# Kernel optimization log

Hardware: AMD Instinct MI355X
Metric: run time of the kernel (lower is better)

Reference implementation:

```python
import jax, jax.numpy as jnp
import numpy as np

IMG, P, D, E, TOPK, H = 224, 14, 512, 10, 2, 8
NP = (IMG // P) ** 2  # 256 patches
PD = P * P            # 196
HID = 256             # expert hidden (hardcoded in source)


def _moe_layer(x, Wip, bip, Wqkv, bqkv, Wo, bo, Wg, bg, W1, b1, W2, b2):
    # input projection (input_dim == adjusted_dim == 512 here)
    h = x @ Wip + bip                                  # [b, s, d]
    b, s, d = h.shape
    hd = d // H
    # torch nn.MultiheadAttention with batch_first=False receives [b, s, d]
    # untransposed -> seq axis is the BATCH axis (l,m below), batch axis is
    # the patch axis (n). Faithfully reproduced.
    qkv = h @ Wqkv + bqkv                              # [b, s, 3d]
    q, k, v = jnp.split(qkv, 3, axis=-1)
    q = q.reshape(b, s, H, hd)
    k = k.reshape(b, s, H, hd)
    v = v.reshape(b, s, H, hd)
    scores = jnp.einsum('lnhd,mnhd->nhlm', q, k) / np.sqrt(hd)
    attn = jax.nn.softmax(scores, axis=-1)             # [s, H, b, b]
    o = jnp.einsum('nhlm,mnhd->lnhd', attn, v).reshape(b, s, d)
    o = o @ Wo + bo                                    # [b, s, d]
    # gating + top-k dispatch
    probs = jax.nn.softmax(o @ Wg + bg, axis=-1)       # [b, s, E]
    topv, topi = jax.lax.top_k(probs, TOPK)
    topv = topv / jnp.sum(topv, axis=-1, keepdims=True)
    # combine weights per (token, expert): [b, s, E]
    w = jnp.sum(jax.nn.one_hot(topi, E, dtype=o.dtype) * topv[..., None], axis=2)
    # expert MLPs (dense over experts, weighted combine == masked scatter-add)
    h1 = jax.nn.relu(jnp.einsum('bsd,edh->bseh', o, W1) + b1)   # [b, s, E, HID]
    out = jnp.einsum('bseh,eho,bse->bso', h1, W2, w) \
        + jnp.einsum('bse,eo->bso', w, b2)
    return out


def _patchify(x):
    # x: [b, 1, IMG, IMG] -> [b, NP, PD]  (unfold/unfold/permute in source)
    b = x.shape[0]
    n = IMG // P
    x = x.reshape(b, n, P, n, P)
    x = x.transpose(0, 1, 3, 2, 4)
    return x.reshape(b, n * n, PD)


def _moe_params(key, prefix):
    ks = jax.random.split(key, 12)
    g = lambda k, shape: jax.random.normal(k, shape, jnp.float32) * 0.02
    return {
        prefix + 'Wip': g(ks[0], (D, D)),   prefix + 'bip': jnp.zeros((D,), jnp.float32),
        prefix + 'Wqkv': g(ks[1], (D, 3 * D)), prefix + 'bqkv': jnp.zeros((3 * D,), jnp.float32),
        prefix + 'Wo': g(ks[2], (D, D)),    prefix + 'bo': jnp.zeros((D,), jnp.float32),
        prefix + 'Wg': g(ks[3], (D, E)),    prefix + 'bg': jnp.zeros((E,), jnp.float32),
        prefix + 'W1': g(ks[4], (E, D, HID)), prefix + 'b1': jnp.zeros((E, HID), jnp.float32),
        prefix + 'W2': g(ks[5], (E, HID, D)), prefix + 'b2': jnp.zeros((E, D), jnp.float32),
    }


def setup_inputs() -> dict:
    key = jax.random.key(0)
    ks = jax.random.split(key, 8)
    g = lambda k, shape: jax.random.normal(k, shape, jnp.float32) * 0.02
    inp = {'x': jax.random.normal(ks[0], (64, 1, IMG, IMG), jnp.float32)}
    inp['pos_emb'] = g(ks[1], (1, NP, D))
    inp['Wp'] = g(ks[2], (PD, D))
    inp['bp'] = jnp.zeros((D,), jnp.float32)
    inp.update(_moe_params(ks[3], 'm1_'))
    inp.update(_moe_params(ks[4], 'm2_'))
    inp['Wv'] = g(ks[5], (D, D))
    inp['bv'] = jnp.zeros((D,), jnp.float32)
    inp['Wc'] = g(ks[6], (D, D))
    inp['bc'] = jnp.zeros((D,), jnp.float32)
    return inp


def reference(x, pos_emb, Wp, bp,
              m1_Wip, m1_bip, m1_Wqkv, m1_bqkv, m1_Wo, m1_bo, m1_Wg, m1_bg,
              m1_W1, m1_b1, m1_W2, m1_b2,
              m2_Wip, m2_bip, m2_Wqkv, m2_bqkv, m2_Wo, m2_bo, m2_Wg, m2_bg,
              m2_W1, m2_b1, m2_W2, m2_b2,
              Wv, bv, Wc, bc):
    tok = _patchify(x) @ Wp + bp + pos_emb             # [b, NP, D]
    first = _moe_layer(tok, m1_Wip, m1_bip, m1_Wqkv, m1_bqkv, m1_Wo, m1_bo,
                       m1_Wg, m1_bg, m1_W1, m1_b1, m1_W2, m1_b2)
    first_vec = first @ Wv + bv
    second = _moe_layer(first_vec, m2_Wip, m2_bip, m2_Wqkv, m2_bqkv, m2_Wo, m2_bo,
                        m2_Wg, m2_bg, m2_W1, m2_b1, m2_W2, m2_b2)
    second_vec = second @ Wv + bv
    cls_first = first @ Wc + bc
    cls_second = second @ Wc + bc
    return (first_vec, second_vec, cls_first, cls_second)
```

## Files before the change

kernel.cpp:

```cpp
#include <hip/hip_runtime.h>
#include <cstdint>
#include <cstddef>

typedef _Float16 half_t;
typedef _Float16 h8 __attribute__((ext_vector_type(8)));
typedef float f4 __attribute__((ext_vector_type(4)));

static constexpr int TOKENS = 16384;
static constexpr int DIM    = 512;
static constexpr int NEXP   = 10;
static constexpr int EHID   = 256;
static constexpr int ECAP   = 4096;
static constexpr float LSC  = 4096.f;
static constexpr float LSCI = 1.f / 4096.f;

__device__ __forceinline__ void split_hl(float v, half_t& h, half_t& l) {
  h = (half_t)v;
  l = (half_t)((v - (float)h) * LSC);
}

__global__ __launch_bounds__(256) void k_wprep(const float* __restrict__ W,
                                               half_t* __restrict__ Ohi,
                                               half_t* __restrict__ Olo,
                                               int K, int N, int KP)
{
  __shared__ float T[32][33];
  const int z = blockIdx.z;
  W   += (size_t)z * K * N;
  Ohi += (size_t)z * N * KP;
  Olo += (size_t)z * N * KP;
  const int t = threadIdx.x;
  const int bn = blockIdx.x * 32, bk = blockIdx.y * 32;
  {
    int nl = t & 31, kq = t >> 5;
#pragma unroll
    for (int i = 0; i < 4; ++i) {
      int kl = kq + i * 8;
      int k = bk + kl;
      T[kl][nl] = (k < K) ? W[(size_t)k * N + bn + nl] : 0.f;
    }
  }
  __syncthreads();
  {
    int kl = t & 31, nq = t >> 5;
#pragma unroll
    for (int i = 0; i < 4; ++i) {
      int nl = nq + i * 8;
      half_t h, l; split_hl(T[kl][nl], h, l);
      size_t o = (size_t)(bn + nl) * KP + bk + kl;
      Ohi[o] = h; Olo[o] = l;
    }
  }
}

__global__ __launch_bounds__(256) void k_patchify(const float* __restrict__ x,
                                                  half_t* __restrict__ Phi,
                                                  half_t* __restrict__ Plo)
{
  int gid = blockIdx.x * 256 + threadIdx.x;
  if (gid >= TOKENS * 224) return;
  int tk = gid / 224, p = gid - tk * 224;
  float v = 0.f;
  if (p < 196) {
    int b = tk >> 8, n = tk & 255;
    int ni = n >> 4, nj = n & 15;
    int pi = p / 14, pj = p - pi * 14;
    v = x[(size_t)b * 50176 + (size_t)(ni * 14 + pi) * 224 + (nj * 14 + pj)];
  }
  half_t h, l; split_hl(v, h, l);
  Phi[gid] = h; Plo[gid] = l;
}

template <int EPI>
__global__ __launch_bounds__(256) void k_mgemm(
    const half_t* __restrict__ Ahi, const half_t* __restrict__ Alo,
    const half_t* __restrict__ Bhi, const half_t* __restrict__ Blo,
    const float* __restrict__ bias, const float* __restrict__ pos,
    float* __restrict__ Cf, half_t* __restrict__ Chi, half_t* __restrict__ Clo,
    int K, int Cld)
{
  __shared__ half_t Ah[128][40], Al[128][40], Bh[128][40], Bl[128][40];
  const int tid = threadIdx.x;
  const int row0 = blockIdx.x * 128;
  const int col0 = blockIdx.y * 128;
  const int lane = tid & 63, wid = tid >> 6;
  const int wm = wid & 1, wn = wid >> 1;
  const int l16 = lane & 15, lq = lane >> 4;
  f4 acc1[4][4], acc2[4][4];
#pragma unroll
  for (int a = 0; a < 4; ++a)
#pragma unroll
    for (int b = 0; b < 4; ++b) {
      acc1[a][b] = {0.f, 0.f, 0.f, 0.f};
      acc2[a][b] = {0.f, 0.f, 0.f, 0.f};
    }
  for (int k0 = 0; k0 < K; k0 += 32) {
#pragma unroll
    for (int i = 0; i < 2; ++i) {
      int lin = tid + i * 256;
      int r = lin >> 2, kc = (lin & 3) << 3;
      const size_t ga = (size_t)(row0 + r) * K + k0 + kc;
      *(uint4*)&Ah[r][kc] = *(const uint4*)&Ahi[ga];
      *(uint4*)&Al[r][kc] = *(const uint4*)&Alo[ga];
      const size_t gb = (size_t)(col0 + r) * K + k0 + kc;
      *(uint4*)&Bh[r][kc] = *(const uint4*)&Bhi[gb];
      *(uint4*)&Bl[r][kc] = *(const uint4*)&Blo[gb];
    }
    __syncthreads();
    h8 ah[4], al2[4];
#pragma unroll
    for (int mt = 0; mt < 4; ++mt) {
      int r = wm * 64 + mt * 16 + l16;
      ah[mt]  = *(const h8*)&Ah[r][lq * 8];
      al2[mt] = *(const h8*)&Al[r][lq * 8];
    }
#pragma unroll
    for (int nt = 0; nt < 4; ++nt) {
      int rb = wn * 64 + nt * 16 + l16;
      h8 bh = *(const h8*)&Bh[rb][lq * 8];
      h8 bl = *(const h8*)&Bl[rb][lq * 8];
#pragma unroll
      for (int mt = 0; mt < 4; ++mt) {
        acc1[mt][nt] = __builtin_amdgcn_mfma_f32_16x16x32_f16(ah[mt], bh, acc1[mt][nt], 0, 0, 0);
        acc2[mt][nt] = __builtin_amdgcn_mfma_f32_16x16x32_f16(ah[mt], bl, acc2[mt][nt], 0, 0, 0);
        acc2[mt][nt] = __builtin_amdgcn_mfma_f32_16x16x32_f16(al2[mt], bh, acc2[mt][nt], 0, 0, 0);
      }
    }
    __syncthreads();
  }
#pragma unroll
  for (int mt = 0; mt < 4; ++mt) {
#pragma unroll
    for (int nt = 0; nt < 4; ++nt) {
      const int col = col0 + wn * 64 + nt * 16 + l16;
      const float bv = bias[col];
#pragma unroll
      for (int r = 0; r < 4; ++r) {
        const int row = row0 + wm * 64 + mt * 16 + lq * 4 + r;
        float v = acc1[mt][nt][r] + acc2[mt][nt][r] * LSCI + bv;
        if (EPI == 0) v += pos[(size_t)(row & 255) * 512 + col];
        const size_t ci = (size_t)row * Cld + col;
        if (EPI == 2 || EPI == 3) Cf[ci] = v;
        if (EPI == 0 || EPI == 1 || EPI == 3) {
          half_t h, l; split_hl(v, h, l);
          Chi[ci] = h; Clo[ci] = l;
        }
      }
    }
  }
}

__global__ __launch_bounds__(256) void k_attn(const float* __restrict__ qkv,
                                              half_t* __restrict__ oHi,
                                              half_t* __restrict__ oLo)
{
  __shared__ float Qs[64][68];
  __shared__ float Ks[64][68];
  __shared__ float Vs[64][68];
  const int n = blockIdx.x;
  const int h = blockIdx.y;
  const int tid = threadIdx.x;
  const int l = tid >> 2, q = tid & 3;
  {
    const float* rowp = qkv + (size_t)(l * 256 + n) * 1536 + h * 64;
#pragma unroll
    for (int i = 0; i < 4; ++i) {
      int c = q * 16 + i * 4;
      *(float4*)&Qs[l][c] = *(const float4*)(rowp + c);
      *(float4*)&Ks[l][c] = *(const float4*)(rowp + 512 + c);
      *(float4*)&Vs[l][c] = *(const float4*)(rowp + 1024 + c);
    }
  }
  __syncthreads();
  float s[16];
#pragma unroll
  for (int j = 0; j < 16; ++j) {
    int m = (j << 2) + q;
    float a = 0.f;
#pragma unroll
    for (int k4 = 0; k4 < 16; ++k4) {
      float4 qa = *(const float4*)&Qs[l][k4 * 4];
      float4 kb = *(const float4*)&Ks[m][k4 * 4];
      a = fmaf(qa.x, kb.x, a); a = fmaf(qa.y, kb.y, a);
      a = fmaf(qa.z, kb.z, a); a = fmaf(qa.w, kb.w, a);
    }
    s[j] = a * 0.125f;
  }
  float mx = s[0];
#pragma unroll
  for (int j = 1; j < 16; ++j) mx = fmaxf(mx, s[j]);
  mx = fmaxf(mx, __shfl_xor(mx, 1));
  mx = fmaxf(mx, __shfl_xor(mx, 2));
  float sum = 0.f;
#pragma unroll
  for (int j = 0; j < 16; ++j) { s[j] = expf(s[j] - mx); sum += s[j]; }
  sum += __shfl_xor(sum, 1);
  sum += __shfl_xor(sum, 2);
  float inv = 1.f / sum;
  __syncthreads();
#pragma unroll
  for (int j = 0; j < 16; ++j) Qs[l][(j << 2) + q] = s[j] * inv;
  __syncthreads();
  float av[16] = {};
  for (int m = 0; m < 64; ++m) {
    float p = Qs[l][m];
#pragma unroll
    for (int i = 0; i < 4; ++i) {
      float4 v4 = *(const float4*)&Vs[m][q * 16 + i * 4];
      av[i * 4 + 0] = fmaf(p, v4.x, av[i * 4 + 0]);
      av[i * 4 + 1] = fmaf(p, v4.y, av[i * 4 + 1]);
      av[i * 4 + 2] = fmaf(p, v4.z, av[i * 4 + 2]);
      av[i * 4 + 3] = fmaf(p, v4.w, av[i * 4 + 3]);
    }
  }
  const size_t base = (size_t)(l * 256 + n) * 512 + h * 64 + q * 16;
  h8 hv0, hv1, lv0, lv1;
#pragma unroll
  for (int i = 0; i < 8; ++i) { half_t hh, ll; split_hl(av[i], hh, ll); hv0[i] = hh; lv0[i] = ll; }
#pragma unroll
  for (int i = 0; i < 8; ++i) { half_t hh, ll; split_hl(av[8 + i], hh, ll); hv1[i] = hh; lv1[i] = ll; }
  *(h8*)&oHi[base] = hv0; *(h8*)&oHi[base + 8] = hv1;
  *(h8*)&oLo[base] = lv0; *(h8*)&oLo[base + 8] = lv1;
}

__global__ __launch_bounds__(256) void k_gate(const float* __restrict__ o2,
                                              const float* __restrict__ Wg,
                                              const float* __restrict__ bg,
                                              int2* __restrict__ tok_e,
                                              float2* __restrict__ tok_w)
{
  const int wave = threadIdx.x >> 6;
  const int lane = threadIdx.x & 63;
  const int t = blockIdx.x * 4 + wave;
  const float* xr = o2 + (size_t)t * DIM;
  float acc[NEXP];
#pragma unroll
  for (int e = 0; e < NEXP; ++e) acc[e] = 0.f;
#pragma unroll
  for (int i = 0; i < 8; ++i) {
    int d = i * 64 + lane;
    float xv = xr[d];
    const float* wr = Wg + (size_t)d * NEXP;
#pragma unroll
    for (int e = 0; e < NEXP; ++e) acc[e] = fmaf(xv, wr[e], acc[e]);
  }
#pragma unroll
  for (int e = 0; e < NEXP; ++e) {
    float v = acc[e];
    v += __shfl_xor(v, 32); v += __shfl_xor(v, 16); v += __shfl_xor(v, 8);
    v += __shfl_xor(v, 4);  v += __shfl_xor(v, 2);  v += __shfl_xor(v, 1);
    acc[e] = v;
  }
  if (lane == 0) {
    float p[NEXP];
    float mx = -1e30f;
#pragma unroll
    for (int e = 0; e < NEXP; ++e) { p[e] = acc[e] + bg[e]; mx = fmaxf(mx, p[e]); }
#pragma unroll
    for (int e = 0; e < NEXP; ++e) p[e] = expf(p[e] - mx);
    int i0 = 0;
#pragma unroll
    for (int e = 1; e < NEXP; ++e) if (p[e] > p[i0]) i0 = e;
    int i1 = (i0 == 0) ? 1 : 0;
#pragma unroll
    for (int e = 0; e < NEXP; ++e)
      if (e != i0 && e != i1 && p[e] > p[i1]) i1 = e;
    float wsum = p[i0] + p[i1];
    tok_e[t] = make_int2(i0, i1);
    tok_w[t] = make_float2(p[i0] / wsum, p[i1] / wsum);
  }
}

__global__ __launch_bounds__(256) void k_scatter(const int2* __restrict__ tok_e,
                                                 const float2* __restrict__ tok_w,
                                                 int* __restrict__ counts,
                                                 int* __restrict__ lt,
                                                 float* __restrict__ lw)
{
  __shared__ int lcnt[32];
  __shared__ int lbase[32];
  const int tid = threadIdx.x;
  if (tid < 32) lcnt[tid] = 0;
  __syncthreads();
  const int t = blockIdx.x * 256 + tid;
  int2 e = tok_e[t];
  float2 w = tok_w[t];
  int s0 = atomicAdd(&lcnt[e.x], 1);
  int s1 = atomicAdd(&lcnt[16 + e.y], 1);
  __syncthreads();
  if (tid < 32) lbase[tid] = atomicAdd(&counts[tid], lcnt[tid]);
  __syncthreads();
  int i0 = lbase[e.x] + s0;
  int i1 = lbase[16 + e.y] + s1;
  if (i0 < ECAP) { int p = e.x * ECAP + i0;            lt[p] = t; lw[p] = w.x; }
  if (i1 < ECAP) { int p = (10 + e.y) * ECAP + i1;     lt[p] = t; lw[p] = w.y; }
}

template <int MODE>
__global__ __launch_bounds__(256) void k_mexpert(
    const float* __restrict__ Af32,
    const half_t* __restrict__ BhiAll, const half_t* __restrict__ BloAll,
    const float* __restrict__ biasAll,
    const int* __restrict__ counts, const int* __restrict__ lt,
    const float* __restrict__ lw,
    float* __restrict__ Hout, half_t* __restrict__ Dhi, half_t* __restrict__ Dlo,
    int K, int N)
{
  const int z = blockIdx.z;
  int slot, e;
  if (MODE == 0) { slot = z / 10; e = z - slot * 10; }
  else           { slot = MODE - 1; e = z; }
  const int cnt = counts[slot * 16 + e];
  const int i0 = blockIdx.x * 64;
  if (i0 >= cnt) return;
  const int col0 = blockIdx.y * 64;
  __shared__ half_t Ah[64][40], Al[64][40], Bh[64][40], Bl[64][40];
  __shared__ int rows[64];
  __shared__ float wts[64];
  const int tid = threadIdx.x;
  if (tid < 64) {
    int i = i0 + tid;
    rows[tid] = (i < cnt) ? lt[(slot * 10 + e) * ECAP + i] : -1;
    wts[tid]  = (i < cnt) ? lw[(slot * 10 + e) * ECAP + i] : 0.f;
  }
  __syncthreads();
  const half_t* Bhi = BhiAll + (size_t)e * K * N;
  const half_t* Blo = BloAll + (size_t)e * K * N;
  const int lane = tid & 63, wid = tid >> 6;
  const int wm = wid & 1, wn = wid >> 1;
  const int l16 = lane & 15, lq = lane >> 4;
  f4 acc1[2][2], acc2[2][2];
#pragma unroll
  for (int a = 0; a < 2; ++a)
#pragma unroll
    for (int b = 0; b < 2; ++b) {
      acc1[a][b] = {0.f, 0.f, 0.f, 0.f};
      acc2[a][b] = {0.f, 0.f, 0.f, 0.f};
    }
  const int sr = tid >> 2;
  const int sc = (tid & 3) << 3;
  for (int k0 = 0; k0 < K; k0 += 32) {
    {
      int trow = rows[sr];
      float4 v0 = make_float4(0.f, 0.f, 0.f, 0.f), v1 = v0;
      if (trow >= 0) {
        size_t ar = (MODE == 0) ? (size_t)trow : (size_t)(trow * 2 + slot);
        const float* ap = Af32 + ar * K + k0 + sc;
        v0 = *(const float4*)ap;
        v1 = *(const float4*)(ap + 4);
      }
      h8 hh, ll;
      float vv[8] = {v0.x, v0.y, v0.z, v0.w, v1.x, v1.y, v1.z, v1.w};
#pragma unroll
      for (int i = 0; i < 8; ++i) { half_t a, b; split_hl(vv[i], a, b); hh[i] = a; ll[i] = b; }
      *(h8*)&Ah[sr][sc] = hh;
      *(h8*)&Al[sr][sc] = ll;
    }
    {
      const size_t gb = (size_t)(col0 + sr) * K + k0 + sc;
      *(uint4*)&Bh[sr][sc] = *(const uint4*)&Bhi[gb];
      *(uint4*)&Bl[sr][sc] = *(const uint4*)&Blo[gb];
    }
    __syncthreads();
    h8 ah[2], al2[2], bh[2], bl[2];
#pragma unroll
    for (int mt = 0; mt < 2; ++mt) {
      int r = wm * 32 + mt * 16 + l16;
      ah[mt]  = *(const h8*)&Ah[r][lq * 8];
      al2[mt] = *(const h8*)&Al[r][lq * 8];
    }
#pragma unroll
    for (int nt = 0; nt < 2; ++nt) {
      int r = wn * 32 + nt * 16 + l16;
      bh[nt] = *(const h8*)&Bh[r][lq * 8];
      bl[nt] = *(const h8*)&Bl[r][lq * 8];
    }
#pragma unroll
    for (int mt = 0; mt < 2; ++mt)
#pragma unroll
      for (int nt = 0; nt < 2; ++nt) {
        acc1[mt][nt] = __builtin_amdgcn_mfma_f32_16x16x32_f16(ah[mt], bh[nt], acc1[mt][nt], 0, 0, 0);
        acc2[mt][nt] = __builtin_amdgcn_mfma_f32_16x16x32_f16(ah[mt], bl[nt], acc2[mt][nt], 0, 0, 0);
        acc2[mt][nt] = __builtin_amdgcn_mfma_f32_16x16x32_f16(al2[mt], bh[nt], acc2[mt][nt], 0, 0, 0);
      }
    __syncthreads();
  }
#pragma unroll
  for (int mt = 0; mt < 2; ++mt) {
#pragma unroll
    for (int nt = 0; nt < 2; ++nt) {
      const int col = col0 + wn * 32 + nt * 16 + l16;
      const float bv = biasAll[(size_t)e * N + col];
#pragma unroll
      for (int r = 0; r < 4; ++r) {
        const int ridx = wm * 32 + mt * 16 + lq * 4 + r;
        const int trow = rows[ridx];
        if (trow < 0) continue;
        float v = acc1[mt][nt][r] + acc2[mt][nt][r] * LSCI;
        if (MODE == 0) {
          float o = fmaxf(v + bv, 0.f);
          Hout[(size_t)(trow * 2 + slot) * N + col] = o;
        } else {
          float o = wts[ridx] * (v + bv);
          const size_t di = (size_t)trow * N + col;
          if (MODE == 2) o += (float)Dhi[di] + (float)Dlo[di] * LSCI;
          half_t h, l; split_hl(o, h, l);
          Dhi[di] = h; Dlo[di] = l;
        }
      }
    }
  }
}

__global__ void k_zero(int* counts)
{
  if (threadIdx.x < 32) counts[threadIdx.x] = 0;
}

extern "C" void kernel_launch(void* const* d_in, const int* in_sizes, int n_in,
                              void* d_out, int out_size, void* d_ws, size_t ws_size,
                              hipStream_t stream)
{
  const float* x   = (const float*)d_in[0];
  const float* pos = (const float*)d_in[1];
  const float* Wp  = (const float*)d_in[2];
  const float* bp  = (const float*)d_in[3];
  const float* w1p[12];
  const float* w2p[12];
  for (int i = 0; i < 12; ++i) {
    w1p[i] = (const float*)d_in[4 + i];
    w2p[i] = (const float*)d_in[16 + i];
  }
  const float* Wv = (const float*)d_in[28];
  const float* bv = (const float*)d_in[29];
  const float* Wc = (const float*)d_in[30];
  const float* bc = (const float*)d_in[31];

  const size_t MiB = 1ull << 20;
  char* wsb = (char*)d_ws;

  half_t* wbase = (half_t*)wsb;
  size_t woff = 0;
  auto walloc = [&](size_t n) { half_t* p = wbase + woff; woff += n; return p; };
  half_t* wpT_hi = walloc(512 * 224);
  half_t* wpT_lo = walloc(512 * 224);
  struct LayerW {
    half_t *wip_h, *wip_l, *wqkv_h, *wqkv_l, *wo_h, *wo_l, *w1_h, *w1_l, *w2_h, *w2_l;
  } lw_[2];
  for (int L = 0; L < 2; ++L) {
    lw_[L].wip_h  = walloc(512 * 512);       lw_[L].wip_l  = walloc(512 * 512);
    lw_[L].wqkv_h = walloc(1536 * 512);      lw_[L].wqkv_l = walloc(1536 * 512);
    lw_[L].wo_h   = walloc(512 * 512);       lw_[L].wo_l   = walloc(512 * 512);
    lw_[L].w1_h   = walloc(10 * 256 * 512);  lw_[L].w1_l   = walloc(10 * 256 * 512);
    lw_[L].w2_h   = walloc(10 * 512 * 256);  lw_[L].w2_l   = walloc(10 * 512 * 256);
  }
  half_t* wvT_hi = walloc(512 * 512);
  half_t* wvT_lo = walloc(512 * 512);
  half_t* wcT_hi = walloc(512 * 512);
  half_t* wcT_lo = walloc(512 * 512);

  char* sm = wsb + 33 * MiB;
  int*    counts = (int*)sm;
  int*    lt     = (int*)(sm + 1024);
  float*  lwt    = (float*)(sm + 1024 + 327680);
  int2*   tok_e  = (int2*)(sm + 1024 + 655360);
  float2* tok_w  = (float2*)(sm + 1024 + 655360 + 131072);

  char* RA = wsb + 34 * MiB;
  char* RB = wsb + 66 * MiB;
  char* RD = wsb + 98 * MiB;
  char* RQ = wsb + 130 * MiB;
  half_t* tokHi = (half_t*)RA;          half_t* tokLo = (half_t*)(RA + 16 * MiB);
  float*  H1    = (float*)RA;
  half_t* fvHi  = (half_t*)RA;          half_t* fvLo  = (half_t*)(RA + 16 * MiB);
  half_t* hHi   = (half_t*)RB;          half_t* hLo   = (half_t*)(RB + 16 * MiB);
  float*  o2    = (float*)RB;
  half_t* atHi  = (half_t*)RD;          half_t* atLo  = (half_t*)(RD + 16 * MiB);
  half_t* dstHi = (half_t*)RD;          half_t* dstLo = (half_t*)(RD + 16 * MiB);
  half_t* PHi   = (half_t*)RQ;          half_t* PLo   = (half_t*)(RQ + 8 * MiB);
  float*  qkvf  = (float*)RQ;

  float* out0 = (float*)d_out;
  float* out1 = out0 + 8388608;
  float* out2 = out0 + 16777216;
  float* out3 = out0 + 25165824;

  k_wprep<<<dim3(16, 7, 1),  dim3(256), 0, stream>>>(Wp, wpT_hi, wpT_lo, 196, 512, 224);
  for (int L = 0; L < 2; ++L) {
    const float* const* w = (L == 0) ? w1p : w2p;
    k_wprep<<<dim3(16, 16, 1),  dim3(256), 0, stream>>>(w[0], lw_[L].wip_h,  lw_[L].wip_l,  512, 512, 512);
    k_wprep<<<dim3(48, 16, 1),  dim3(256), 0, stream>>>(w[2], lw_[L].wqkv_h, lw_[L].wqkv_l, 512, 1536, 512);
    k_wprep<<<dim3(16, 16, 1),  dim3(256), 0, stream>>>(w[4], lw_[L].wo_h,   lw_[L].wo_l,   512, 512, 512);
    k_wprep<<<dim3(8, 16, 10),  dim3(256), 0, stream>>>(w[8], lw_[L].w1_h,   lw_[L].w1_l,   512, 256, 512);
    k_wprep<<<dim3(16, 8, 10),  dim3(256), 0, stream>>>(w[10], lw_[L].w2_h,  lw_[L].w2_l,   256, 512, 256);
  }
  k_wprep<<<dim3(16, 16, 1), dim3(256), 0, stream>>>(Wv, wvT_hi, wvT_lo, 512, 512, 512);
  k_wprep<<<dim3(16, 16, 1), dim3(256), 0, stream>>>(Wc, wcT_hi, wcT_lo, 512, 512, 512);

  k_patchify<<<dim3(14336), dim3(256), 0, stream>>>(x, PHi, PLo);
  k_mgemm<0><<<dim3(128, 4), dim3(256), 0, stream>>>(
      PHi, PLo, wpT_hi, wpT_lo, bp, pos, nullptr, tokHi, tokLo, 224, 512);

  auto moe = [&](int L, const half_t* inHi, const half_t* inLo) {
    const LayerW& W = lw_[L];
    const float* const* w = (L == 0) ? w1p : w2p;
    k_zero<<<dim3(1), dim3(64), 0, stream>>>(counts);
    k_mgemm<1><<<dim3(128, 4), dim3(256), 0, stream>>>(
        inHi, inLo, W.wip_h, W.wip_l, w[1], nullptr, nullptr, hHi, hLo, 512, 512);
    k_mgemm<2><<<dim3(128, 12), dim3(256), 0, stream>>>(
        hHi, hLo, W.wqkv_h, W.wqkv_l, w[3], nullptr, qkvf, nullptr, nullptr, 512, 1536);
    k_attn<<<dim3(256, 8), dim3(256), 0, stream>>>(qkvf, atHi, atLo);
    k_mgemm<2><<<dim3(128, 4), dim3(256), 0, stream>>>(
        atHi, atLo, W.wo_h, W.wo_l, w[5], nullptr, o2, nullptr, nullptr, 512, 512);
    k_gate<<<dim3(4096), dim3(256), 0, stream>>>(o2, w[6], w[7], tok_e, tok_w);
    k_scatter<<<dim3(64), dim3(256), 0, stream>>>(tok_e, tok_w, counts, lt, lwt);
    k_mexpert<0><<<dim3(64, 4, 20), dim3(256), 0, stream>>>(
        o2, W.w1_h, W.w1_l, w[9], counts, lt, lwt, H1, nullptr, nullptr, 512, 256);
    k_mexpert<1><<<dim3(64, 8, 10), dim3(256), 0, stream>>>(
        H1, W.w2_h, W.w2_l, w[11], counts, lt, lwt, nullptr, dstHi, dstLo, 256, 512);
    k_mexpert<2><<<dim3(64, 8, 10), dim3(256), 0, stream>>>(
        H1, W.w2_h, W.w2_l, w[11], counts, lt, lwt, nullptr, dstHi, dstLo, 256, 512);
  };

  moe(0, tokHi, tokLo);
  k_mgemm<3><<<dim3(128, 4), dim3(256), 0, stream>>>(
      dstHi, dstLo, wvT_hi, wvT_lo, bv, nullptr, out0, fvHi, fvLo, 512, 512);
  k_mgemm<2><<<dim3(128, 4), dim3(256), 0, stream>>>(
      dstHi, dstLo, wcT_hi, wcT_lo, bc, nullptr, out2, nullptr, nullptr, 512, 512);
  moe(1, fvHi, fvLo);
  k_mgemm<2><<<dim3(128, 4), dim3(256), 0, stream>>>(
      dstHi, dstLo, wvT_hi, wvT_lo, bv, nullptr, out1, nullptr, nullptr, 512, 512);
  k_mgemm<2><<<dim3(128, 4), dim3(256), 0, stream>>>(
      dstHi, dstLo, wcT_hi, wcT_lo, bc, nullptr, out3, nullptr, nullptr, 512, 512);
}
```

Before: 1.542 ms.

## Use direct global-to-LDS loads, narrow GEMM tiles, and fuse Wv/Wc projections

Loads of the GEMM and expert-GEMM operand tiles now use global_load_lds 16-byte copies, which bypass registers, in place of staging through uint4 register copies. The GEMM output tile shrinks from 128x128 to 128x64, which doubles the grid and lowers accumulator register pressure. The Wv and Wc weights are concatenated into one 1024-wide matrix so that each pair of output projections runs as a single GEMM with a split epilogue. The LDS layout loses its padding (stride 32 instead of 40), which may add bank conflicts on the fragment reads.

```diff
diff --git a/kernel.cpp b/kernel.cpp
--- a/kernel.cpp
+++ b/kernel.cpp
@@ -9,7 +9,6 @@
 static constexpr int TOKENS = 16384;
 static constexpr int DIM    = 512;
 static constexpr int NEXP   = 10;
-static constexpr int EHID   = 256;
 static constexpr int ECAP   = 4096;
 static constexpr float LSC  = 4096.f;
 static constexpr float LSCI = 1.f / 4096.f;
@@ -17,6 +16,12 @@
 __device__ __forceinline__ void split_hl(float v, half_t& h, half_t& l) {
   h = (half_t)v;
   l = (half_t)((v - (float)h) * LSC);
+}
+
+__device__ __forceinline__ void gld16(const void* g, void* l) {
+  __builtin_amdgcn_global_load_lds(
+      (const __attribute__((address_space(1))) uint32_t*)g,
+      (__attribute__((address_space(3))) uint32_t*)l, 16, 0, 0);
 }
 
 __global__ __launch_bounds__(256) void k_wprep(const float* __restrict__ W,
@@ -75,50 +80,59 @@
 __global__ __launch_bounds__(256) void k_mgemm(
     const half_t* __restrict__ Ahi, const half_t* __restrict__ Alo,
     const half_t* __restrict__ Bhi, const half_t* __restrict__ Blo,
-    const float* __restrict__ bias, const float* __restrict__ pos,
-    float* __restrict__ Cf, half_t* __restrict__ Chi, half_t* __restrict__ Clo,
+    const float* __restrict__ bias, const float* __restrict__ bias2,
+    const float* __restrict__ pos,
+    float* __restrict__ Cf, float* __restrict__ Cf2,
+    half_t* __restrict__ Chi, half_t* __restrict__ Clo,
     int K, int Cld)
 {
-  __shared__ half_t Ah[128][40], Al[128][40], Bh[128][40], Bl[128][40];
+  __shared__ __align__(16) half_t AhL[128 * 32];
+  __shared__ __align__(16) half_t AlL[128 * 32];
+  __shared__ __align__(16) half_t BhL[64 * 32];
+  __shared__ __align__(16) half_t BlL[64 * 32];
   const int tid = threadIdx.x;
   const int row0 = blockIdx.x * 128;
-  const int col0 = blockIdx.y * 128;
+  const int col0 = blockIdx.y * 64;
   const int lane = tid & 63, wid = tid >> 6;
   const int wm = wid & 1, wn = wid >> 1;
   const int l16 = lane & 15, lq = lane >> 4;
-  f4 acc1[4][4], acc2[4][4];
+  const int srA = lane >> 2;
+  const int scA = (lane & 3) << 3;
+  f4 acc1[4][2], acc2[4][2];
 #pragma unroll
   for (int a = 0; a < 4; ++a)
 #pragma unroll
-    for (int b = 0; b < 4; ++b) {
+    for (int b = 0; b < 2; ++b) {
       acc1[a][b] = {0.f, 0.f, 0.f, 0.f};
       acc2[a][b] = {0.f, 0.f, 0.f, 0.f};
     }
   for (int k0 = 0; k0 < K; k0 += 32) {
 #pragma unroll
-    for (int i = 0; i < 2; ++i) {
-      int lin = tid + i * 256;
-      int r = lin >> 2, kc = (lin & 3) << 3;
-      const size_t ga = (size_t)(row0 + r) * K + k0 + kc;
-      *(uint4*)&Ah[r][kc] = *(const uint4*)&Ahi[ga];
-      *(uint4*)&Al[r][kc] = *(const uint4*)&Alo[ga];
-      const size_t gb = (size_t)(col0 + r) * K + k0 + kc;
-      *(uint4*)&Bh[r][kc] = *(const uint4*)&Bhi[gb];
-      *(uint4*)&Bl[r][kc] = *(const uint4*)&Blo[gb];
+    for (int c = 0; c < 2; ++c) {
+      const int r0 = wid * 32 + c * 16;
+      const size_t ga = (size_t)(row0 + r0 + srA) * K + k0 + scA;
+      gld16(&Ahi[ga], &AhL[r0 * 32]);
+      gld16(&Alo[ga], &AlL[r0 * 32]);
+    }
+    {
+      const int r0 = wid * 16;
+      const size_t gb = (size_t)(col0 + r0 + srA) * K + k0 + scA;
+      gld16(&Bhi[gb], &BhL[r0 * 32]);
+      gld16(&Blo[gb], &BlL[r0 * 32]);
     }
     __syncthreads();
     h8 ah[4], al2[4];
 #pragma unroll
     for (int mt = 0; mt < 4; ++mt) {
       int r = wm * 64 + mt * 16 + l16;
-      ah[mt]  = *(const h8*)&Ah[r][lq * 8];
-      al2[mt] = *(const h8*)&Al[r][lq * 8];
-    }
-#pragma unroll
-    for (int nt = 0; nt < 4; ++nt) {
-      int rb = wn * 64 + nt * 16 + l16;
-      h8 bh = *(const h8*)&Bh[rb][lq * 8];
-      h8 bl = *(const h8*)&Bl[rb][lq * 8];
+      ah[mt]  = *(const h8*)&AhL[r * 32 + lq * 8];
+      al2[mt] = *(const h8*)&AlL[r * 32 + lq * 8];
+    }
+#pragma unroll
+    for (int nt = 0; nt < 2; ++nt) {
+      int rb = wn * 32 + nt * 16 + l16;
+      h8 bh = *(const h8*)&BhL[rb * 32 + lq * 8];
+      h8 bl = *(const h8*)&BlL[rb * 32 + lq * 8];
 #pragma unroll
       for (int mt = 0; mt < 4; ++mt) {
         acc1[mt][nt] = __builtin_amdgcn_mfma_f32_16x16x32_f16(ah[mt], bh, acc1[mt][nt], 0, 0, 0);
@@ -131,19 +145,31 @@
 #pragma unroll
   for (int mt = 0; mt < 4; ++mt) {
 #pragma unroll
-    for (int nt = 0; nt < 4; ++nt) {
-      const int col = col0 + wn * 64 + nt * 16 + l16;
-      const float bv = bias[col];
+    for (int nt = 0; nt < 2; ++nt) {
+      const int col = col0 + wn * 32 + nt * 16 + l16;
+      float bvv;
+      if (EPI == 4 || EPI == 5) bvv = (col < 512) ? bias[col] : bias2[col - 512];
+      else                      bvv = bias[col];
 #pragma unroll
       for (int r = 0; r < 4; ++r) {
         const int row = row0 + wm * 64 + mt * 16 + lq * 4 + r;
-        float v = acc1[mt][nt][r] + acc2[mt][nt][r] * LSCI + bv;
+        float v = acc1[mt][nt][r] + acc2[mt][nt][r] * LSCI + bvv;
         if (EPI == 0) v += pos[(size_t)(row & 255) * 512 + col];
-        const size_t ci = (size_t)row * Cld + col;
-        if (EPI == 2 || EPI == 3) Cf[ci] = v;
-        if (EPI == 0 || EPI == 1 || EPI == 3) {
-          half_t h, l; split_hl(v, h, l);
-          Chi[ci] = h; Clo[ci] = l;
+        if (EPI == 4 || EPI == 5) {
+          if (col < 512) {
+            const size_t ci = (size_t)row * 512 + col;
+            Cf[ci] = v;
+            if (EPI == 4) { half_t h, l; split_hl(v, h, l); Chi[ci] = h; Clo[ci] = l; }
+          } else {
+            Cf2[(size_t)row * 512 + col - 512] = v;
+          }
+        } else {
+          const size_t ci = (size_t)row * Cld + col;
+          if (EPI == 2 || EPI == 3) Cf[ci] = v;
+          if (EPI == 0 || EPI == 1 || EPI == 3) {
+            half_t h, l; split_hl(v, h, l);
+            Chi[ci] = h; Clo[ci] = l;
+          }
         }
       }
     }
@@ -314,7 +340,8 @@
   const int i0 = blockIdx.x * 64;
   if (i0 >= cnt) return;
   const int col0 = blockIdx.y * 64;
-  __shared__ half_t Ah[64][40], Al[64][40], Bh[64][40], Bl[64][40];
+  __shared__ __align__(16) half_t Ah[64][40], Al[64][40];
+  __shared__ __align__(16) half_t BhL[64 * 32], BlL[64 * 32];
   __shared__ int rows[64];
   __shared__ float wts[64];
   const int tid = threadIdx.x;
@@ -329,6 +356,8 @@
   const int lane = tid & 63, wid = tid >> 6;
   const int wm = wid & 1, wn = wid >> 1;
   const int l16 = lane & 15, lq = lane >> 4;
+  const int srA = lane >> 2;
+  const int scA = (lane & 3) << 3;
   f4 acc1[2][2], acc2[2][2];
 #pragma unroll
   for (int a = 0; a < 2; ++a)
@@ -340,6 +369,12 @@
   const int sr = tid >> 2;
   const int sc = (tid & 3) << 3;
   for (int k0 = 0; k0 < K; k0 += 32) {
+    {
+      const int r0 = wid * 16;
+      const size_t gb = (size_t)(col0 + r0 + srA) * K + k0 + scA;
+      gld16(&Bhi[gb], &BhL[r0 * 32]);
+      gld16(&Blo[gb], &BlL[r0 * 32]);
+    }
     {
       int trow = rows[sr];
       float4 v0 = make_float4(0.f, 0.f, 0.f, 0.f), v1 = v0;
@@ -356,11 +391,6 @@
       *(h8*)&Ah[sr][sc] = hh;
       *(h8*)&Al[sr][sc] = ll;
     }
-    {
-      const size_t gb = (size_t)(col0 + sr) * K + k0 + sc;
-      *(uint4*)&Bh[sr][sc] = *(const uint4*)&Bhi[gb];
-      *(uint4*)&Bl[sr][sc] = *(const uint4*)&Blo[gb];
-    }
     __syncthreads();
     h8 ah[2], al2[2], bh[2], bl[2];
 #pragma unroll
@@ -372,8 +402,8 @@
 #pragma unroll
     for (int nt = 0; nt < 2; ++nt) {
       int r = wn * 32 + nt * 16 + l16;
-      bh[nt] = *(const h8*)&Bh[r][lq * 8];
-      bl[nt] = *(const h8*)&Bl[r][lq * 8];
+      bh[nt] = *(const h8*)&BhL[r * 32 + lq * 8];
+      bl[nt] = *(const h8*)&BlL[r * 32 + lq * 8];
     }
 #pragma unroll
     for (int mt = 0; mt < 2; ++mt)
@@ -454,10 +484,8 @@
     lw_[L].w1_h   = walloc(10 * 256 * 512);  lw_[L].w1_l   = walloc(10 * 256 * 512);
     lw_[L].w2_h   = walloc(10 * 512 * 256);  lw_[L].w2_l   = walloc(10 * 512 * 256);
   }
-  half_t* wvT_hi = walloc(512 * 512);
-  half_t* wvT_lo = walloc(512 * 512);
-  half_t* wcT_hi = walloc(512 * 512);
-  half_t* wcT_lo = walloc(512 * 512);
+  half_t* wvcT_hi = walloc(1024 * 512);
+  half_t* wvcT_lo = walloc(1024 * 512);
 
   char* sm = wsb + 33 * MiB;
   int*    counts = (int*)sm;
@@ -494,24 +522,28 @@
     k_wprep<<<dim3(8, 16, 10),  dim3(256), 0, stream>>>(w[8], lw_[L].w1_h,   lw_[L].w1_l,   512, 256, 512);
     k_wprep<<<dim3(16, 8, 10),  dim3(256), 0, stream>>>(w[10], lw_[L].w2_h,  lw_[L].w2_l,   256, 512, 256);
   }
-  k_wprep<<<dim3(16, 16, 1), dim3(256), 0, stream>>>(Wv, wvT_hi, wvT_lo, 512, 512, 512);
-  k_wprep<<<dim3(16, 16, 1), dim3(256), 0, stream>>>(Wc, wcT_hi, wcT_lo, 512, 512, 512);
+  k_wprep<<<dim3(16, 16, 1), dim3(256), 0, stream>>>(Wv, wvcT_hi, wvcT_lo, 512, 512, 512);
+  k_wprep<<<dim3(16, 16, 1), dim3(256), 0, stream>>>(Wc, wvcT_hi + 512 * 512,
+                                                     wvcT_lo + 512 * 512, 512, 512, 512);
 
   k_patchify<<<dim3(14336), dim3(256), 0, stream>>>(x, PHi, PLo);
-  k_mgemm<0><<<dim3(128, 4), dim3(256), 0, stream>>>(
-      PHi, PLo, wpT_hi, wpT_lo, bp, pos, nullptr, tokHi, tokLo, 224, 512);
+  k_mgemm<0><<<dim3(128, 8), dim3(256), 0, stream>>>(
+      PHi, PLo, wpT_hi, wpT_lo, bp, nullptr, pos, nullptr, nullptr, tokHi, tokLo, 224, 512);
 
   auto moe = [&](int L, const half_t* inHi, const half_t* inLo) {
     const LayerW& W = lw_[L];
     const float* const* w = (L == 0) ? w1p : w2p;
     k_zero<<<dim3(1), dim3(64), 0, stream>>>(counts);
-    k_mgemm<1><<<dim3(128, 4), dim3(256), 0, stream>>>(
-        inHi, inLo, W.wip_h, W.wip_l, w[1], nullptr, nullptr, hHi, hLo, 512, 512);
-    k_mgemm<2><<<dim3(128, 12), dim3(256), 0, stream>>>(
-        hHi, hLo, W.wqkv_h, W.wqkv_l, w[3], nullptr, qkvf, nullptr, nullptr, 512, 1536);
+    k_mgemm<1><<<dim3(128, 8), dim3(256), 0, stream>>>(
+        inHi, inLo, W.wip_h, W.wip_l, w[1], nullptr, nullptr, nullptr, nullptr,
+        hHi, hLo, 512, 512);
+    k_mgemm<2><<<dim3(128, 24), dim3(256), 0, stream>>>(
+        hHi, hLo, W.wqkv_h, W.wqkv_l, w[3], nullptr, nullptr, qkvf, nullptr,
+        nullptr, nullptr, 512, 1536);
     k_attn<<<dim3(256, 8), dim3(256), 0, stream>>>(qkvf, atHi, atLo);
-    k_mgemm<2><<<dim3(128, 4), dim3(256), 0, stream>>>(
-        atHi, atLo, W.wo_h, W.wo_l, w[5], nullptr, o2, nullptr, nullptr, 512, 512);
+    k_mgemm<2><<<dim3(128, 8), dim3(256), 0, stream>>>(
+        atHi, atLo, W.wo_h, W.wo_l, w[5], nullptr, nullptr, o2, nullptr,
+        nullptr, nullptr, 512, 512);
     k_gate<<<dim3(4096), dim3(256), 0, stream>>>(o2, w[6], w[7], tok_e, tok_w);
     k_scatter<<<dim3(64), dim3(256), 0, stream>>>(tok_e, tok_w, counts, lt, lwt);
     k_mexpert<0><<<dim3(64, 4, 20), dim3(256), 0, stream>>>(
@@ -523,13 +555,9 @@
   };
 
   moe(0, tokHi, tokLo);
-  k_mgemm<3><<<dim3(128, 4), dim3(256), 0, stream>>>(
-      dstHi, dstLo, wvT_hi, wvT_lo, bv, nullptr, out0, fvHi, fvLo, 512, 512);
-  k_mgemm<2><<<dim3(128, 4), dim3(256), 0, stream>>>(
-      dstHi, dstLo, wcT_hi, wcT_lo, bc, nullptr, out2, nullptr, nullptr, 512, 512);
+  k_mgemm<4><<<dim3(128, 16), dim3(256), 0, stream>>>(
+      dstHi, dstLo, wvcT_hi, wvcT_lo, bv, bc, nullptr, out0, out2, fvHi, fvLo, 512, 512);
   moe(1, fvHi, fvLo);
-  k_mgemm<2><<<dim3(128, 4), dim3(256), 0, stream>>>(
-      dstHi, dstLo, wvT_hi, wvT_lo, bv, nullptr, out1, nullptr, nullptr, 512, 512);
-  k_mgemm<2><<<dim3(128, 4), dim3(256), 0, stream>>>(
-      dstHi, dstLo, wcT_hi, wcT_lo, bc, nullptr, out3, nullptr, nullptr, 512, 512);
-}
+  k_mgemm<5><<<dim3(128, 16), dim3(256), 0, stream>>>(
+      dstHi, dstLo, wvcT_hi, wvcT_lo, bv, bc, nullptr, out1, out3, nullptr, nullptr, 512, 512);
+}
```

Result: faster. 1.316 ms (-14.7%).
